# Kernel optimization log

Hardware: AMD Instinct MI355X
Metric: run time of the kernel (lower is better)

## Reference

```python
import jax, jax.numpy as jnp
import numpy as np


def _entmax15(x):
    """Entmax 1.5 over the last axis, matching the TF GRANDE implementation.

    x: [..., K] logits. Returns activations of same shape summing to 1 over -1.
    """
    x = x / 2.0
    x = x - jnp.max(x, axis=-1, keepdims=True)
    # full descending sort (same heuristic as original: top_k with k = K)
    xs = -jnp.sort(-x, axis=-1)                      # [..., K] descending
    K = x.shape[-1]
    rho = jnp.arange(1, K + 1, dtype=x.dtype)        # 1..K
    mean = jnp.cumsum(xs, axis=-1) / rho
    mean_sq = jnp.cumsum(xs * xs, axis=-1) / rho
    delta = (1.0 - rho * (mean_sq - mean * mean)) / rho
    tau = mean - jnp.sqrt(jax.nn.relu(delta))        # candidate thresholds
    support = jnp.sum((tau <= xs).astype(jnp.int32), axis=-1, keepdims=True)
    tau_star = jnp.take_along_axis(tau, support - 1, axis=-1)
    y_sqrt = jax.nn.relu(x - tau_star)
    return y_sqrt * y_sqrt


def setup_inputs() -> dict:
    key = jax.random.key(0)
    # [n_estimators, internal_nodes, n_features] feature-selection logits
    logits = jax.random.normal(key, (2048, 127, 256), dtype=jnp.float32)
    return {"logits": logits}


def reference(logits):
    return _entmax15(logits)
```

## Files before the change

### kernel.cpp

```cpp
#include <hip/hip_runtime.h>


#define K 256
#define NITER 6

typedef float vf4 __attribute__((ext_vector_type(4)));

__device__ __forceinline__ void load_batch(const float* __restrict__ p,
                                           float x[16]) {
    #pragma unroll
    for (int k = 0; k < 4; ++k) {
        const vf4 v = *reinterpret_cast<const vf4*>(p + k * 64);
        x[k*4+0] = v.x; x[k*4+1] = v.y; x[k*4+2] = v.z; x[k*4+3] = v.w;
    }
}

__device__ __forceinline__ void load_batch_nt(const float* __restrict__ p,
                                              float x[16]) {
    #pragma unroll
    for (int k = 0; k < 4; ++k) {
        const vf4 v = __builtin_nontemporal_load(
            reinterpret_cast<const vf4*>(p + k * 64));
        x[k*4+0] = v.x; x[k*4+1] = v.y; x[k*4+2] = v.z; x[k*4+3] = v.w;
    }
}

__device__ __forceinline__ void solve_store(const float x[16],
                                            float* __restrict__ op) {
    float m0 = fmaxf(x[0], x[1]);
    float m1 = fmaxf(x[2], x[3]);
    float m2 = fmaxf(x[4], x[5]);
    float m3 = fmaxf(x[6], x[7]);
    #pragma unroll
    for (int i = 8; i < 16; i += 4) {
        m0 = fmaxf(m0, x[i+0]);
        m1 = fmaxf(m1, x[i+1]);
        m2 = fmaxf(m2, x[i+2]);
        m3 = fmaxf(m3, x[i+3]);
    }
    float m = fmaxf(fmaxf(m0, m1), fmaxf(m2, m3));
    m = fmaxf(m, __shfl_xor(m, 1, 64));
    m = fmaxf(m, __shfl_xor(m, 2, 64));
    m = fmaxf(m, __shfl_xor(m, 4, 64));
    m = fmaxf(m, __shfl_xor(m, 8, 64));

    float t = m - 2.0f;
    #pragma unroll
    for (int it = 0; it < NITER; ++it) {
        float s1a = 0.0f, s1b = 0.0f, s2a = 0.0f, s2b = 0.0f;
        #pragma unroll
        for (int i = 0; i < 16; i += 2) {
            const float d0 = fmaxf(x[i]   - t, 0.0f);
            const float d1 = fmaxf(x[i+1] - t, 0.0f);
            s1a += d0;
            s1b += d1;
            s2a = fmaf(d0, d0, s2a);
            s2b = fmaf(d1, d1, s2b);
        }
        float s1 = s1a + s1b;
        float s2 = s2a + s2b;
        s1 += __shfl_xor(s1, 1, 64);
        s2 += __shfl_xor(s2, 1, 64);
        s1 += __shfl_xor(s1, 2, 64);
        s2 += __shfl_xor(s2, 2, 64);
        s1 += __shfl_xor(s1, 4, 64);
        s2 += __shfl_xor(s2, 4, 64);
        s1 += __shfl_xor(s1, 8, 64);
        s2 += __shfl_xor(s2, 8, 64);
        t += (s2 - 4.0f) * 0.5f * __builtin_amdgcn_rcpf(s1);
    }

    #pragma unroll
    for (int k = 0; k < 4; ++k) {
        const float d0 = fmaxf(x[k*4+0] - t, 0.0f) * 0.5f;
        const float d1 = fmaxf(x[k*4+1] - t, 0.0f) * 0.5f;
        const float d2 = fmaxf(x[k*4+2] - t, 0.0f) * 0.5f;
        const float d3 = fmaxf(x[k*4+3] - t, 0.0f) * 0.5f;
        vf4 v;
        v.x = d0 * d0;
        v.y = d1 * d1;
        v.z = d2 * d2;
        v.w = d3 * d3;
        __builtin_nontemporal_store(v, reinterpret_cast<vf4*>(op + k * 64));
    }
}

__global__ __launch_bounds__(256) void entmax15_kernel(
    const float* __restrict__ in, float* __restrict__ out, int nwaves)
{
    const int lane = threadIdx.x & 63;
    const int wave = threadIdx.x >> 6;
    const int sub  = lane & 15;
    const int rloc = lane >> 4;
    const int g    = blockIdx.x * 4 + wave;

    const long long base    = ((long long)g * 4 + rloc) * K + sub * 4;
    const long long bstride = (long long)nwaves * 4 * K;
    const long long off0 = base;
    const long long off1 = base + bstride;
    const long long off2 = base + 2 * bstride;
    const long long off3 = base + 3 * bstride;

    float xA[16], xB[16];

    load_batch(in + off0, xA);
    __builtin_amdgcn_sched_barrier(0);
    load_batch(in + off1, xB);
    __builtin_amdgcn_sched_barrier(0);

    solve_store(xA, out + off0);

    load_batch(in + off2, xA);
    __builtin_amdgcn_sched_barrier(0);

    solve_store(xB, out + off1);

    load_batch_nt(in + off3, xB);
    __builtin_amdgcn_sched_barrier(0);

    solve_store(xA, out + off2);
    solve_store(xB, out + off3);
}

extern "C" void kernel_launch(void* const* d_in, const int* in_sizes, int n_in,
                              void* d_out, int out_size, void* d_ws, size_t ws_size,
                              hipStream_t stream)
{
    const float* in = (const float*)d_in[0];
    float* out = (float*)d_out;
    const int nrows  = in_sizes[0] / K;
    const int nwaves = nrows / (4 * 4);
    const int blocks = nwaves / 4;
    entmax15_kernel<<<dim3(blocks), dim3(256), 0, stream>>>(in, out, nwaves);
}
```

Before: 81.80 us.

## Stage input through LDS with async global_load_lds double buffering

Input loads now go through global_load_lds DMA into per-wave double-buffered shared memory, with manual vmcnt waits, in place of register loads. This lets up to two batches be in flight without holding registers, which should give deeper prefetch and better latency hiding. The cost is an extra LDS read per batch, 32KB of LDS per block (which may limit occupancy), and hand-tuned waitcnt values. The vmcnt values count stores too, so they may be subtly off and risk reading data before it arrives.

```diff
diff --git a/kernel.cpp b/kernel.cpp
--- a/kernel.cpp
+++ b/kernel.cpp
@@ -6,21 +6,21 @@
 
 typedef float vf4 __attribute__((ext_vector_type(4)));
 
-__device__ __forceinline__ void load_batch(const float* __restrict__ p,
-                                           float x[16]) {
+#define WAITV(n) asm volatile("s_waitcnt vmcnt(" #n ")" ::: "memory")
+#define WAITLGKM0 asm volatile("s_waitcnt lgkmcnt(0)" ::: "memory")
+
+__device__ __forceinline__ void dma_batch(const float* gp, float* lp) {
     #pragma unroll
     for (int k = 0; k < 4; ++k) {
-        const vf4 v = *reinterpret_cast<const vf4*>(p + k * 64);
-        x[k*4+0] = v.x; x[k*4+1] = v.y; x[k*4+2] = v.z; x[k*4+3] = v.w;
+        __builtin_amdgcn_global_load_lds(gp + k * 64, lp + k * 256, 16, 0, 0);
     }
 }
 
-__device__ __forceinline__ void load_batch_nt(const float* __restrict__ p,
-                                              float x[16]) {
+__device__ __forceinline__ void lds_read(const float* lp, int rloc, int sub,
+                                         float x[16]) {
     #pragma unroll
     for (int k = 0; k < 4; ++k) {
-        const vf4 v = __builtin_nontemporal_load(
-            reinterpret_cast<const vf4*>(p + k * 64));
+        const vf4 v = *reinterpret_cast<const vf4*>(lp + k * 256 + rloc * 64 + sub * 4);
         x[k*4+0] = v.x; x[k*4+1] = v.y; x[k*4+2] = v.z; x[k*4+3] = v.w;
     }
 }
@@ -88,6 +88,8 @@
 __global__ __launch_bounds__(256) void entmax15_kernel(
     const float* __restrict__ in, float* __restrict__ out, int nwaves)
 {
+    __shared__ float smem[4][2][1024];
+
     const int lane = threadIdx.x & 63;
     const int wave = threadIdx.x >> 6;
     const int sub  = lane & 15;
@@ -95,31 +97,35 @@
     const int g    = blockIdx.x * 4 + wave;
 
     const long long base    = ((long long)g * 4 + rloc) * K + sub * 4;
-    const long long bstride = (long long)nwaves * 4 * K;
-    const long long off0 = base;
-    const long long off1 = base + bstride;
-    const long long off2 = base + 2 * bstride;
-    const long long off3 = base + 3 * bstride;
+    const long long bs      = (long long)nwaves * 4 * K;
 
-    float xA[16], xB[16];
+    float* buf0 = &smem[wave][0][0];
+    float* buf1 = &smem[wave][1][0];
+    const float* gin = in + base;
+    float x[16];
 
-    load_batch(in + off0, xA);
-    __builtin_amdgcn_sched_barrier(0);
-    load_batch(in + off1, xB);
-    __builtin_amdgcn_sched_barrier(0);
+    dma_batch(gin,          buf0);
+    dma_batch(gin + bs,     buf1);
 
-    solve_store(xA, out + off0);
+    WAITV(4);
+    lds_read(buf0, rloc, sub, x);
+    WAITLGKM0;
+    dma_batch(gin + 2 * bs, buf0);
+    solve_store(x, out + base);
 
-    load_batch(in + off2, xA);
-    __builtin_amdgcn_sched_barrier(0);
+    WAITV(8);
+    lds_read(buf1, rloc, sub, x);
+    WAITLGKM0;
+    dma_batch(gin + 3 * bs, buf1);
+    solve_store(x, out + base + bs);
 
-    solve_store(xB, out + off1);
+    WAITV(12);
+    lds_read(buf0, rloc, sub, x);
+    solve_store(x, out + base + 2 * bs);
 
-    load_batch_nt(in + off3, xB);
-    __builtin_amdgcn_sched_barrier(0);
-
-    solve_store(xA, out + off2);
-    solve_store(xB, out + off3);
+    WAITV(8);
+    lds_read(buf1, rloc, sub, x);
+    solve_store(x, out + base + 3 * bs);
 }
 
 extern "C" void kernel_launch(void* const* d_in, const int* in_sizes, int n_in,
```

New measurement: 81.87 us. Within noise of the previous version (+0.1%).
